# Kernel tuning notes

Measured on AMD Instinct MI355X. Metric: run time of the kernel, lower is better.

## Reference

```python
import jax, jax.numpy as jnp
import numpy as np

NUM_EMBEDDINGS = 1024
EMBEDDING_DIM = 256
COMMITMENT_COST = 0.25
B, D, T = 32, 256, 2048


def setup_inputs() -> dict:
    key = jax.random.key(0)
    k1, k2 = jax.random.split(key)
    inputs = jax.random.normal(k1, (B, D, T), dtype=jnp.float32)
    # nn.Embedding weight init: uniform(-1/K, 1/K)
    embeddings = jax.random.uniform(
        k2, (NUM_EMBEDDINGS, EMBEDDING_DIM), dtype=jnp.float32,
        minval=-1.0 / NUM_EMBEDDINGS, maxval=1.0 / NUM_EMBEDDINGS)
    return {"inputs": inputs, "embeddings": embeddings}


def reference(inputs, embeddings):
    # [B, D, T] -> [B, T, D]
    x = jnp.transpose(inputs, (0, 2, 1))
    Bs, Ts, Ds = x.shape
    flat = x.reshape(-1, Ds)  # [N, D]
    # squared L2 distances to each codebook entry: [N, K]
    distances = (jnp.sum(flat ** 2, axis=1, keepdims=True)
                 + jnp.sum(embeddings ** 2, axis=1)
                 - 2.0 * flat @ embeddings.T)
    encoding_indices = jnp.argmin(distances, axis=1)  # [N]
    # gather codebook rows (equivalent to one-hot @ embeddings)
    quantized = jnp.take(embeddings, encoding_indices, axis=0).reshape(x.shape)
    e_latent_loss = jnp.mean((jax.lax.stop_gradient(quantized) - x) ** 2)
    q_latent_loss = jnp.mean((quantized - jax.lax.stop_gradient(x)) ** 2)
    loss = q_latent_loss + COMMITMENT_COST * e_latent_loss
    # straight-through estimator
    quantized = x + jax.lax.stop_gradient(quantized - x)
    quantized = jnp.transpose(quantized, (0, 2, 1))  # back to [B, D, T]
    return quantized, loss, encoding_indices.reshape(Bs, Ts)
```

## Files before the change

### kernel.cpp

```cpp
#include <hip/hip_runtime.h>
#include <math.h>

#define K_CODES 1024
#define DIM 256
#define BB 32
#define TT 2048
#define NROWS (BB * TT)
#define QN (BB * DIM * TT)
#define LOSS_OFF QN
#define IDX_OFF (QN + 1)

#define WS_E2 0
#define WS_SX 1024
#define WS_LOSS (1024 + NROWS)

__device__ __forceinline__ float pw128_sq(const float* p, int stride) {
    float r[8];
#pragma unroll
    for (int j = 0; j < 8; ++j) {
        float v = p[j * stride];
        r[j] = __fmul_rn(v, v);
    }
#pragma unroll
    for (int i = 8; i < 128; i += 8) {
#pragma unroll
        for (int j = 0; j < 8; ++j) {
            float v = p[(i + j) * stride];
            r[j] = __fadd_rn(r[j], __fmul_rn(v, v));
        }
    }
    return __fadd_rn(__fadd_rn(__fadd_rn(r[0], r[1]), __fadd_rn(r[2], r[3])),
                     __fadd_rn(__fadd_rn(r[4], r[5]), __fadd_rn(r[6], r[7])));
}

__device__ __forceinline__ float pw256_sq(const float* p, int stride) {
    return __fadd_rn(pw128_sq(p, stride), pw128_sq(p + 128 * stride, stride));
}

__global__ void k_prep_e2(const float* __restrict__ emb, float* __restrict__ ws) {
    int k = blockIdx.x * 256 + threadIdx.x;
    if (k == 0) ws[WS_LOSS] = 0.0f;
    if (k < K_CODES) ws[WS_E2 + k] = pw256_sq(emb + (size_t)k * DIM, 1);
}

__global__ void k_prep_sx(const float* __restrict__ in, float* __restrict__ ws) {
    int row = blockIdx.x * 256 + threadIdx.x;
    int b = row >> 11;
    int t = row & (TT - 1);
    ws[WS_SX + row] = pw256_sq(in + (size_t)b * (DIM * TT) + t, TT);
}

__launch_bounds__(256, 2)
__global__ void k_main(const float* __restrict__ in, const float* __restrict__ emb,
                       const float* __restrict__ ws, float* __restrict__ wloss,
                       float* __restrict__ out) {
    __shared__ float smem[8192];
    __shared__ int idx_lds[128];
    float* xs = smem;
    float* es = smem + 4096;

    const int tid = threadIdx.x;
    const int tx = tid & 15;
    const int ty = tid >> 4;
    const int row0 = blockIdx.x * 128;
    const int b = row0 >> 11;
    const int t0 = row0 & (TT - 1);
    const float* xbase = in + (size_t)b * (DIM * TT) + t0;

    float sxr[8];
#pragma unroll
    for (int i = 0; i < 8; ++i) sxr[i] = ws[WS_SX + row0 + 8 * ty + i];

    float bestd[8];
    int bestidx[8];
#pragma unroll
    for (int i = 0; i < 8; ++i) { bestd[i] = INFINITY; bestidx[i] = 0; }

    const int lr = tid & 127;
    const int lh = tid >> 7;

    for (int cc = 0; cc < 8; ++cc) {
        const int cbase = cc * 128;
        float acc[8][8];
#pragma unroll
        for (int i = 0; i < 8; ++i)
#pragma unroll
            for (int j = 0; j < 8; ++j) acc[i][j] = 0.0f;

        for (int dc = 0; dc < 8; ++dc) {
            const int d0 = dc * 32;
            __syncthreads();
#pragma unroll
            for (int it = 0; it < 4; ++it) {
                int c4 = lh + 2 * it;
                float v0 = xbase[(size_t)(d0 + 4 * c4 + 0) * TT + lr];
                float v1 = xbase[(size_t)(d0 + 4 * c4 + 1) * TT + lr];
                float v2 = xbase[(size_t)(d0 + 4 * c4 + 2) * TT + lr];
                float v3 = xbase[(size_t)(d0 + 4 * c4 + 3) * TT + lr];
                int cs = c4 ^ ((lr >> 3) & 7);
                *(float4*)&xs[lr * 32 + cs * 4] = make_float4(v0, v1, v2, v3);
            }
#pragma unroll
            for (int it = 0; it < 4; ++it) {
                int s = tid + 256 * it;
                int code = s >> 3;
                int c4 = s & 7;
                float4 v = *(const float4*)&emb[(size_t)(cbase + code) * DIM + d0 + c4 * 4];
                int cs = c4 ^ ((code >> 3) & 7);
                *(float4*)&es[code * 32 + cs * 4] = v;
            }
            __syncthreads();
#pragma unroll
            for (int c4 = 0; c4 < 8; ++c4) {
                float4 xv[8], ev[8];
                const int xc = (c4 ^ (ty & 7)) * 4;
                const int ec = (c4 ^ (tx & 7)) * 4;
#pragma unroll
                for (int i = 0; i < 8; ++i) xv[i] = *(const float4*)&xs[(8 * ty + i) * 32 + xc];
#pragma unroll
                for (int j = 0; j < 8; ++j) ev[j] = *(const float4*)&es[(8 * tx + j) * 32 + ec];
#pragma unroll
                for (int i = 0; i < 8; ++i)
#pragma unroll
                    for (int j = 0; j < 8; ++j) {
                        float a = acc[i][j];
                        a = __fmaf_rn(xv[i].x, ev[j].x, a);
                        a = __fmaf_rn(xv[i].y, ev[j].y, a);
                        a = __fmaf_rn(xv[i].z, ev[j].z, a);
                        a = __fmaf_rn(xv[i].w, ev[j].w, a);
                        acc[i][j] = a;
                    }
            }
        }
#pragma unroll
        for (int j = 0; j < 8; ++j) {
            const int code = cbase + 8 * tx + j;
            const float e2 = ws[WS_E2 + code];
#pragma unroll
            for (int i = 0; i < 8; ++i) {
                float dist = __fsub_rn(__fadd_rn(sxr[i], e2), __fmul_rn(2.0f, acc[i][j]));
                if (dist < bestd[i]) { bestd[i] = dist; bestidx[i] = code; }
            }
        }
    }

    __syncthreads();
    float* rd = smem;
    int* ri = (int*)(smem + 2048);
#pragma unroll
    for (int i = 0; i < 8; ++i) {
        rd[(8 * ty + i) * 16 + tx] = bestd[i];
        ri[(8 * ty + i) * 16 + tx] = bestidx[i];
    }
    __syncthreads();
    if (tid < 128) {
        float bd = rd[tid * 16];
        int bi = ri[tid * 16];
#pragma unroll
        for (int x = 1; x < 16; ++x) {
            float d = rd[tid * 16 + x];
            int ix = ri[tid * 16 + x];
            if (d < bd || (d == bd && ix < bi)) { bd = d; bi = ix; }
        }
        idx_lds[tid] = bi;
        out[IDX_OFF + b * TT + t0 + tid] = (float)bi;
    }
    __syncthreads();

    float lsum = 0.0f;
    float* q = smem;
    const int qr = tid >> 3;
    const int qf = tid & 7;
    const int er_ = tid & 127;
    const int ed_ = tid >> 7;
    for (int dc = 0; dc < 8; ++dc) {
        const int d0 = dc * 32;
        __syncthreads();
#pragma unroll
        for (int it = 0; it < 4; ++it) {
            int r = qr + 32 * it;
            float4 v = *(const float4*)&emb[(size_t)idx_lds[r] * DIM + d0 + qf * 4];
            float* dst = &q[r * 37 + qf * 4];
            dst[0] = v.x; dst[1] = v.y; dst[2] = v.z; dst[3] = v.w;
        }
        __syncthreads();
#pragma unroll
        for (int k = 0; k < 16; ++k) {
            int dd = ed_ + 2 * k;
            float qq = q[er_ * 37 + dd];
            size_t gaddr = (size_t)b * (DIM * TT) + (size_t)(d0 + dd) * TT + t0 + er_;
            float xx = in[gaddr];
            out[gaddr] = qq;
            float df = __fsub_rn(qq, xx);
            lsum = __fmaf_rn(df, df, lsum);
        }
    }
#pragma unroll
    for (int off = 32; off > 0; off >>= 1) lsum += __shfl_down(lsum, off, 64);
    if ((tid & 63) == 0) atomicAdd(wloss, lsum);
}

__global__ void k_loss(const float* __restrict__ wloss, float* __restrict__ out) {
    out[LOSS_OFF] = 1.25f * wloss[0] / 16777216.0f;
}

extern "C" void kernel_launch(void* const* d_in, const int* in_sizes, int n_in,
                              void* d_out, int out_size, void* d_ws, size_t ws_size,
                              hipStream_t stream) {
    const float* in = (const float*)d_in[0];
    const float* emb = (const float*)d_in[1];
    float* out = (float*)d_out;
    float* ws = (float*)d_ws;

    hipLaunchKernelGGL(k_prep_e2, dim3(4), dim3(256), 0, stream, emb, ws);
    hipLaunchKernelGGL(k_prep_sx, dim3(256), dim3(256), 0, stream, in, ws);
    hipLaunchKernelGGL(k_main, dim3(512), dim3(256), 0, stream, in, emb, ws,
                       ws + WS_LOSS, out);
    hipLaunchKernelGGL(k_loss, dim3(1), dim3(1), 0, stream, ws + WS_LOSS, out);
}
```

Measured before the change: 618.4 us.

## Retile main kernel to 64 rows x 256 codes per block with 1024 blocks

Changes the block tile from 128 rows x 128 codes to 64 rows x 256 codes, doubling the grid to 1024 blocks and raising the launch-bounds occupancy hint to 4 blocks per CU. Codebook norms are hoisted into registers per code chunk, and pointer increments replace recomputed addresses in the load loops. The aim is more blocks to fill the 256 CUs and better latency hiding. The cost is that the codebook is now streamed once per 64 rows instead of per 128, and 4 blocks per CU may force register spills given the 64-entry accumulator tile.

```diff
diff --git a/kernel.cpp b/kernel.cpp
--- a/kernel.cpp
+++ b/kernel.cpp
@@ -50,19 +50,18 @@
     ws[WS_SX + row] = pw256_sq(in + (size_t)b * (DIM * TT) + t, TT);
 }
 
-__launch_bounds__(256, 2)
+__launch_bounds__(256, 4)
 __global__ void k_main(const float* __restrict__ in, const float* __restrict__ emb,
                        const float* __restrict__ ws, float* __restrict__ wloss,
                        float* __restrict__ out) {
-    __shared__ float smem[8192];
-    __shared__ int idx_lds[128];
+    __shared__ float smem[10240];
     float* xs = smem;
-    float* es = smem + 4096;
+    float* es = smem + 2048;
 
     const int tid = threadIdx.x;
-    const int tx = tid & 15;
-    const int ty = tid >> 4;
-    const int row0 = blockIdx.x * 128;
+    const int tx = tid & 31;
+    const int ty = tid >> 5;
+    const int row0 = blockIdx.x * 64;
     const int b = row0 >> 11;
     const int t0 = row0 & (TT - 1);
     const float* xbase = in + (size_t)b * (DIM * TT) + t0;
@@ -76,44 +75,57 @@
 #pragma unroll
     for (int i = 0; i < 8; ++i) { bestd[i] = INFINITY; bestidx[i] = 0; }
 
-    const int lr = tid & 127;
-    const int lh = tid >> 7;
-
-    for (int cc = 0; cc < 8; ++cc) {
-        const int cbase = cc * 128;
+    const int lr = tid & 63;
+    const int lh = tid >> 6;
+    const int xswz = (lr >> 3) & 7;
+    const int ec4 = tid & 7;
+    const int ecode0 = tid >> 3;
+
+    for (int cc = 0; cc < 4; ++cc) {
+        const int cbase = cc * 256;
+        const float* estart = emb + (size_t)cbase * DIM;
+
+        float e2r[8];
+#pragma unroll
+        for (int j = 0; j < 8; ++j) e2r[j] = ws[WS_E2 + cbase + 8 * tx + j];
+
         float acc[8][8];
 #pragma unroll
         for (int i = 0; i < 8; ++i)
 #pragma unroll
             for (int j = 0; j < 8; ++j) acc[i][j] = 0.0f;
 
+        const float* xp = xbase;
+        const float* ep = estart;
+
         for (int dc = 0; dc < 8; ++dc) {
-            const int d0 = dc * 32;
             __syncthreads();
 #pragma unroll
-            for (int it = 0; it < 4; ++it) {
-                int c4 = lh + 2 * it;
-                float v0 = xbase[(size_t)(d0 + 4 * c4 + 0) * TT + lr];
-                float v1 = xbase[(size_t)(d0 + 4 * c4 + 1) * TT + lr];
-                float v2 = xbase[(size_t)(d0 + 4 * c4 + 2) * TT + lr];
-                float v3 = xbase[(size_t)(d0 + 4 * c4 + 3) * TT + lr];
-                int cs = c4 ^ ((lr >> 3) & 7);
+            for (int it = 0; it < 2; ++it) {
+                int c4 = lh + 4 * it;
+                float v0 = xp[(size_t)(4 * c4 + 0) * TT + lr];
+                float v1 = xp[(size_t)(4 * c4 + 1) * TT + lr];
+                float v2 = xp[(size_t)(4 * c4 + 2) * TT + lr];
+                float v3 = xp[(size_t)(4 * c4 + 3) * TT + lr];
+                int cs = c4 ^ xswz;
                 *(float4*)&xs[lr * 32 + cs * 4] = make_float4(v0, v1, v2, v3);
             }
-#pragma unroll
-            for (int it = 0; it < 4; ++it) {
-                int s = tid + 256 * it;
-                int code = s >> 3;
-                int c4 = s & 7;
-                float4 v = *(const float4*)&emb[(size_t)(cbase + code) * DIM + d0 + c4 * 4];
-                int cs = c4 ^ ((code >> 3) & 7);
-                *(float4*)&es[code * 32 + cs * 4] = v;
+            {
+                const float* eit = ep + (size_t)ecode0 * DIM + ec4 * 4;
+#pragma unroll
+                for (int it = 0; it < 8; ++it) {
+                    int code = ecode0 + 32 * it;
+                    float4 v = *(const float4*)eit;
+                    int cs = ec4 ^ ((code >> 3) & 7);
+                    *(float4*)&es[code * 32 + cs * 4] = v;
+                    eit += 32 * DIM;
+                }
             }
             __syncthreads();
 #pragma unroll
             for (int c4 = 0; c4 < 8; ++c4) {
                 float4 xv[8], ev[8];
-                const int xc = (c4 ^ (ty & 7)) * 4;
+                const int xc = (c4 ^ ty) * 4;
                 const int ec = (c4 ^ (tx & 7)) * 4;
 #pragma unroll
                 for (int i = 0; i < 8; ++i) xv[i] = *(const float4*)&xs[(8 * ty + i) * 32 + xc];
@@ -131,11 +143,13 @@
                         acc[i][j] = a;
                     }
             }
+            xp += (size_t)32 * TT;
+            ep += 32;
         }
 #pragma unroll
         for (int j = 0; j < 8; ++j) {
             const int code = cbase + 8 * tx + j;
-            const float e2 = ws[WS_E2 + code];
+            const float e2 = e2r[j];
 #pragma unroll
             for (int i = 0; i < 8; ++i) {
                 float dist = __fsub_rn(__fadd_rn(sxr[i], e2), __fmul_rn(2.0f, acc[i][j]));
@@ -147,19 +161,20 @@
     __syncthreads();
     float* rd = smem;
     int* ri = (int*)(smem + 2048);
+    int* idx_lds = (int*)(smem + 4096);
 #pragma unroll
     for (int i = 0; i < 8; ++i) {
-        rd[(8 * ty + i) * 16 + tx] = bestd[i];
-        ri[(8 * ty + i) * 16 + tx] = bestidx[i];
+        rd[(8 * ty + i) * 32 + tx] = bestd[i];
+        ri[(8 * ty + i) * 32 + tx] = bestidx[i];
     }
     __syncthreads();
-    if (tid < 128) {
-        float bd = rd[tid * 16];
-        int bi = ri[tid * 16];
-#pragma unroll
-        for (int x = 1; x < 16; ++x) {
-            float d = rd[tid * 16 + x];
-            int ix = ri[tid * 16 + x];
+    if (tid < 64) {
+        float bd = rd[tid * 32];
+        int bi = ri[tid * 32];
+#pragma unroll
+        for (int x = 1; x < 32; ++x) {
+            float d = rd[tid * 32 + x];
+            int ix = ri[tid * 32 + x];
             if (d < bd || (d == bd && ix < bi)) { bd = d; bi = ix; }
         }
         idx_lds[tid] = bi;
@@ -171,13 +186,13 @@
     float* q = smem;
     const int qr = tid >> 3;
     const int qf = tid & 7;
-    const int er_ = tid & 127;
-    const int ed_ = tid >> 7;
+    const int er_ = tid & 63;
+    const int ed_ = tid >> 6;
     for (int dc = 0; dc < 8; ++dc) {
         const int d0 = dc * 32;
         __syncthreads();
 #pragma unroll
-        for (int it = 0; it < 4; ++it) {
+        for (int it = 0; it < 2; ++it) {
             int r = qr + 32 * it;
             float4 v = *(const float4*)&emb[(size_t)idx_lds[r] * DIM + d0 + qf * 4];
             float* dst = &q[r * 37 + qf * 4];
@@ -185,8 +200,8 @@
         }
         __syncthreads();
 #pragma unroll
-        for (int k = 0; k < 16; ++k) {
-            int dd = ed_ + 2 * k;
+        for (int k = 0; k < 8; ++k) {
+            int dd = ed_ + 4 * k;
             float qq = q[er_ * 37 + dd];
             size_t gaddr = (size_t)b * (DIM * TT) + (size_t)(d0 + dd) * TT + t0 + er_;
             float xx = in[gaddr];
@@ -214,7 +229,7 @@
 
     hipLaunchKernelGGL(k_prep_e2, dim3(4), dim3(256), 0, stream, emb, ws);
     hipLaunchKernelGGL(k_prep_sx, dim3(256), dim3(256), 0, stream, in, ws);
-    hipLaunchKernelGGL(k_main, dim3(512), dim3(256), 0, stream, in, emb, ws,
+    hipLaunchKernelGGL(k_main, dim3(1024), dim3(256), 0, stream, in, emb, ws,
                        ws + WS_LOSS, out);
     hipLaunchKernelGGL(k_loss, dim3(1), dim3(1), 0, stream, ws + WS_LOSS, out);
 }
```

Result: slower. 645.4 us (+4.4%).
